# Kernel tuning notes

Hardware: AMD Instinct MI355X
Metric: run time of the kernel (lower is better)

The kernel has to match this reference:

```python
import jax, jax.numpy as jnp
import numpy as np

V, B, T, E, H = 16384, 64, 256, 128, 1024


def setup_inputs() -> dict:
    key = jax.random.key(0)
    ks = jax.random.split(key, 10)
    inp = {
        'input_data': jax.random.randint(ks[0], (B, T), 0, V, dtype=jnp.int32),
        'targets': jax.random.randint(ks[1], (B, T), 0, V, dtype=jnp.int32),
        'embedding': jax.random.normal(ks[2], (V, E), dtype=jnp.float32) * 0.02,
        # layer 1 GRU (input E, hidden H): gate kernel [E+H, 2H], candidate kernel [E+H, H]
        'W_g1': jax.random.normal(ks[3], (E + H, 2 * H), dtype=jnp.float32) * 0.05,
        'b_g1': jnp.ones((2 * H,), dtype=jnp.float32),  # TF GRUCell gate bias init = 1.0
        'W_c1': jax.random.normal(ks[4], (E + H, H), dtype=jnp.float32) * 0.05,
        'b_c1': jnp.zeros((H,), dtype=jnp.float32),
        # layer 2 GRU (input H, hidden H)
        'W_g2': jax.random.normal(ks[5], (2 * H, 2 * H), dtype=jnp.float32) * 0.05,
        'b_g2': jnp.ones((2 * H,), dtype=jnp.float32),
        'W_c2': jax.random.normal(ks[6], (2 * H, H), dtype=jnp.float32) * 0.05,
        'b_c2': jnp.zeros((H,), dtype=jnp.float32),
        'softmax_w': jax.random.normal(ks[7], (H, V), dtype=jnp.float32) * 1e-4,
        'softmax_b': jnp.zeros((V,), dtype=jnp.float32),
    }
    return inp


def _gru_step(h, x, W_g, b_g, W_c, b_c):
    # TF GRUCell: r,u = sigmoid([x,h] @ W_g + b_g); c = tanh([x, r*h] @ W_c + b_c)
    ru = jax.nn.sigmoid(jnp.concatenate([x, h], axis=-1) @ W_g + b_g)
    r, u = jnp.split(ru, 2, axis=-1)
    c = jnp.tanh(jnp.concatenate([x, r * h], axis=-1) @ W_c + b_c)
    return u * h + (1.0 - u) * c


def reference(input_data, targets, embedding, W_g1, b_g1, W_c1, b_c1,
              W_g2, b_g2, W_c2, b_c2, softmax_w, softmax_b):
    # inference path: is_training=False, so dropout wrappers are identity
    x = embedding[input_data]               # [B, T, E]
    xs = jnp.transpose(x, (1, 0, 2))        # [T, B, E] time-major for scan

    h0 = (jnp.zeros((B, H), x.dtype), jnp.zeros((B, H), x.dtype))

    def step(carry, x_t):
        h1, h2 = carry
        h1 = _gru_step(h1, x_t, W_g1, b_g1, W_c1, b_c1)
        h2 = _gru_step(h2, h1, W_g2, b_g2, W_c2, b_c2)
        return (h1, h2), h2

    _, ys = jax.lax.scan(step, h0, xs)      # ys: [T, B, H]
    out = jnp.transpose(ys, (1, 0, 2)).reshape(-1, H)  # [B*T, H] batch-major flatten

    logits = out @ softmax_w + softmax_b    # [B*T, V]
    logp = jax.nn.log_softmax(logits, axis=-1)
    flat_t = targets.reshape(-1)
    nll = -jnp.take_along_axis(logp, flat_t[:, None], axis=1)[:, 0]
    loss = jnp.mean(nll)
    return logits, loss
```

## Files before the change

### kernel.cpp

```cpp
#include <hip/hip_runtime.h>

typedef __bf16 bf16_t;
typedef __bf16 bf16x8 __attribute__((ext_vector_type(8)));
typedef float f32x4 __attribute__((ext_vector_type(4)));
typedef float f32x2 __attribute__((ext_vector_type(2)));
typedef unsigned u32x4 __attribute__((ext_vector_type(4)));

constexpr int kB = 64, kT = 256, kE = 128, kH = 1024, kV = 16384;
constexpr int kBT = kB * kT;

__device__ __forceinline__ void ld16_sc(const void* p, u32x4& d) {
    asm volatile("global_load_dwordx4 %0, %1, off sc0 sc1" : "=v"(d) : "v"(p));
}
__device__ __forceinline__ void ld8_sc(const void* p, f32x2& d) {
    asm volatile("global_load_dwordx2 %0, %1, off sc0 sc1" : "=v"(d) : "v"(p));
}
__device__ __forceinline__ void ld8_c(const void* p, f32x2& d) {
    asm volatile("global_load_dwordx2 %0, %1, off" : "=v"(d) : "v"(p));
}
__device__ __forceinline__ void st4_sc(void* p, unsigned v) {
    asm volatile("global_store_dword %0, %1, off sc0 sc1" :: "v"(p), "v"(v));
}
__device__ __forceinline__ void st8_sc(void* p, f32x2 v) {
    asm volatile("global_store_dwordx2 %0, %1, off sc0 sc1" :: "v"(p), "v"(v));
}
__device__ __forceinline__ unsigned ld_flag(const unsigned* p) {
    unsigned v;
    asm volatile("global_load_dword %0, %1, off sc0 sc1\n\ts_waitcnt vmcnt(0)"
                 : "=v"(v) : "v"(p) : "memory");
    return v;
}
#define WAITVM(n) asm volatile("s_waitcnt vmcnt(" #n ")" ::: "memory")

#define GL2LDS(gp, lp) __builtin_amdgcn_global_load_lds( \
    (const __attribute__((address_space(1))) void*)(gp), \
    (__attribute__((address_space(3))) void*)(lp), 16, 0, 0)

__device__ __forceinline__ unsigned pack_bf16(float a, float b) {
    union { unsigned u; __bf16 h[2]; } c;
    c.h[0] = (__bf16)a; c.h[1] = (__bf16)b;
    return c.u;
}
__device__ __forceinline__ f32x2 mk2(float a, float b) {
    f32x2 v; v[0] = a; v[1] = b; return v;
}

__global__ void zero_bytes(char* p, size_t n) {
    size_t stride = (size_t)gridDim.x * blockDim.x * 16;
    for (size_t i = ((size_t)blockIdx.x * blockDim.x + threadIdx.x) * 16; i < n; i += stride) {
        uint4 z; z.x = z.y = z.z = z.w = 0;
        *reinterpret_cast<uint4*>(p + i) = z;
    }
}

__global__ void transpose_to_bf16(const float* __restrict__ src, bf16_t* __restrict__ dst,
                                  int R, int C) {
    __shared__ float tile[32][33];
    int c0 = blockIdx.x * 32, r0 = blockIdx.y * 32;
    for (int rr = threadIdx.y; rr < 32; rr += 8)
        tile[rr][threadIdx.x] = src[(size_t)(r0 + rr) * C + c0 + threadIdx.x];
    __syncthreads();
    for (int rr = threadIdx.y; rr < 32; rr += 8)
        dst[(size_t)(c0 + rr) * R + r0 + threadIdx.x] = (bf16_t)tile[threadIdx.x][rr];
}

__global__ __launch_bounds__(256) void embed_gather(const int* __restrict__ ids,
                                                    const float* __restrict__ emb,
                                                    bf16_t* __restrict__ XB) {
    int base = blockIdx.x * 16;
    for (int idx = threadIdx.x; idx < 16 * kE; idx += 256) {
        int r = idx >> 7, k = idx & 127;
        int row = base + r;
        XB[(size_t)row * kE + k] = (bf16_t)emb[(size_t)ids[row] * kE + k];
    }
}

__global__ __launch_bounds__(256) void xpre_gemm(
    const bf16_t* __restrict__ XB, const bf16_t* __restrict__ WT,
    const float* __restrict__ bias, float* __restrict__ Cout, int N) {
    __shared__ __align__(16) char As[128 * 256];
    __shared__ __align__(16) char Bs[128 * 256];
    const int tid = threadIdx.x;
    const int w = tid >> 6, l = tid & 63, lr = l & 15, lk8 = (l >> 4) * 8;
    const int wr = w >> 1, wc = w & 1;
    const size_t row0 = (size_t)blockIdx.y * 128, col0 = (size_t)blockIdx.x * 128;
    for (int c = tid; c < 2048; c += 256) {
        int o = c * 16; int row = o >> 8; int kk = o & 255;
        int dst = (row << 8) + (kk ^ ((row & 7) << 4));
        *reinterpret_cast<bf16x8*>(As + dst) =
            *reinterpret_cast<const bf16x8*>(XB + (row0 + row) * kE + (kk >> 1));
        *reinterpret_cast<bf16x8*>(Bs + dst) =
            *reinterpret_cast<const bf16x8*>(WT + (col0 + row) * kE + (kk >> 1));
    }
    __syncthreads();
    f32x4 acc[4][4] = {};
    #pragma unroll
    for (int ks = 0; ks < 4; ++ks) {
        int kb = (ks * 32 + lk8) * 2;
        bf16x8 af[4], bfv[4];
        #pragma unroll
        for (int mf = 0; mf < 4; ++mf) {
            int r = wr * 64 + mf * 16 + lr;
            af[mf] = *reinterpret_cast<const bf16x8*>(As + (r << 8) + (kb ^ ((r & 7) << 4)));
        }
        #pragma unroll
        for (int nf = 0; nf < 4; ++nf) {
            int r = wc * 64 + nf * 16 + lr;
            bfv[nf] = *reinterpret_cast<const bf16x8*>(Bs + (r << 8) + (kb ^ ((r & 7) << 4)));
        }
        #pragma unroll
        for (int mf = 0; mf < 4; ++mf)
            #pragma unroll
            for (int nf = 0; nf < 4; ++nf)
                acc[mf][nf] = __builtin_amdgcn_mfma_f32_16x16x32_bf16(af[mf], bfv[nf], acc[mf][nf], 0, 0, 0);
    }
    #pragma unroll
    for (int mf = 0; mf < 4; ++mf) {
        size_t row = row0 + wr * 64 + mf * 16 + (l >> 4) * 4;
        #pragma unroll
        for (int nf = 0; nf < 4; ++nf) {
            size_t col = col0 + wc * 64 + nf * 16 + lr;
            float bvl = bias[col];
            #pragma unroll
            for (int i = 0; i < 4; ++i)
                Cout[(row + i) * (size_t)N + col] = acc[mf][nf][i] + bvl;
        }
    }
}

struct PP {
    const bf16_t *WG1HT, *WC1HT, *WG2T, *WC2T;
    const float *XG1, *XC1;
    const float *bg2, *bc2;
    float *H1F, *H2F, *U1, *U2;
    bf16_t *X2, *X2C0, *X2C1, *RH1, *YS;
    unsigned *flags;
};

__device__ __forceinline__ void wait_flags(const unsigned* flags, int base, int cnt,
                                           unsigned tgt, int lane) {
    if ((unsigned)lane < (unsigned)cnt) {
        const unsigned* p = flags + (size_t)(base + lane) * 16;
        while (ld_flag(p) < tgt)
            __builtin_amdgcn_s_sleep(1);
    }
}

template<int RBSH>
__device__ __forceinline__ void mm_part(const bf16_t* __restrict__ A, int astr,
                                        const char* __restrict__ wl, int kbase,
                                        int w, int lr, int lk, f32x4 (&acc)[4][2]) {
    const int kbeg = w * 256;
    const bf16_t* base[4];
    #pragma unroll
    for (int mf = 0; mf < 4; ++mf)
        base[mf] = A + (size_t)(mf * 16 + lr) * astr + kbeg + lk;
    u32x4 buf[4][4];
    #pragma unroll
    for (int pi = 0; pi < 4; ++pi)
        #pragma unroll
        for (int mf = 0; mf < 4; ++mf)
            ld16_sc(base[mf] + pi * 32, buf[pi][mf]);
    #pragma unroll
    for (int ki = 0; ki < 8; ++ki) {
        int rem = 7 - ki; if (rem > 3) rem = 3;
        if (rem == 3)      WAITVM(12);
        else if (rem == 2) WAITVM(8);
        else if (rem == 1) WAITVM(4);
        else               WAITVM(0);
        __builtin_amdgcn_sched_barrier(0);
        #pragma unroll
        for (int nf = 0; nf < 2; ++nf) {
            int rr = nf * 16 + lr;
            int kb = (kbase + kbeg + ki * 32 + lk) * 2;
            bf16x8 wv = *reinterpret_cast<const bf16x8*>(wl + (rr << RBSH) + (kb ^ ((rr & 7) << 4)));
            #pragma unroll
            for (int mf = 0; mf < 4; ++mf)
                acc[mf][nf] = __builtin_amdgcn_mfma_f32_16x16x32_bf16(
                    __builtin_bit_cast(bf16x8, buf[ki & 3][mf]), wv, acc[mf][nf], 0, 0, 0);
        }
        if (ki + 4 < 8) {
            #pragma unroll
            for (int mf = 0; mf < 4; ++mf)
                ld16_sc(base[mf] + (ki + 4) * 32, buf[ki & 3][mf]);
        }
    }
}

__global__ __launch_bounds__(256, 1) void rnn_persistent(PP P) {
    __shared__ __align__(16) char wlds[131072];
    __shared__ float red[4][64][8];
    const int blk = blockIdx.x, tid = threadIdx.x;
    const int w = tid >> 6, l = tid & 63, lr = l & 15, lk = (l >> 4) * 8;
    int grp, idx;
    if (blk < 64)       { grp = 0; idx = blk; }
    else if (blk < 96)  { grp = 1; idx = blk - 64; }
    else if (blk < 160) { grp = 2; idx = blk - 96; }
    else                { grp = 3; idx = blk - 160; }
    const int n0 = idx * 32;
    const int K = (grp < 2) ? 1024 : 2048;
    const int rbsh = (grp < 2) ? 11 : 12;
    const bf16_t* Wsrc = (grp == 0) ? P.WG1HT : (grp == 1) ? P.WC1HT : (grp == 2) ? P.WG2T : P.WC2T;

    for (int c = tid; c < (32 * K * 2) / 16; c += 256) {
        int o = c * 16;
        int row = o >> rbsh;
        int kk = o & ((1 << rbsh) - 1);
        bf16x8 v = *reinterpret_cast<const bf16x8*>(Wsrc + (size_t)(n0 + row) * K + (kk >> 1));
        *reinterpret_cast<bf16x8*>(wlds + (row << rbsh) + (kk ^ ((row & 7) << 4))) = v;
    }
    __syncthreads();

    const unsigned* F = P.flags;
    const int r = tid >> 2, cb = (tid & 3) * 2;
    const bool lowhalf = (n0 < 1024);

    f32x2 bx[4], hreg[4];
    #pragma unroll
    for (int p = 0; p < 4; ++p) {
        hreg[p] = mk2(0.f, 0.f);
        int j = n0 + p * 8 + cb;
        if (grp == 2)      bx[p] = *reinterpret_cast<const f32x2*>(P.bg2 + j);
        else if (grp == 3) bx[p] = *reinterpret_cast<const f32x2*>(P.bc2 + j);
    }

    for (int t = 0; t < kT; ++t) {
        unsigned ut = (unsigned)t;
        bf16_t* x2c = (t & 1) ? P.X2C1 : P.X2C0;
        f32x4 acc[4][2] = {};

        if (grp == 0) {
            if (t) wait_flags(F, 64, 32, ut, tid);
            __syncthreads();
            mm_part<11>(P.X2, 2048, wlds, 0, w, lr, lk, acc);
        } else if (grp == 1) {
            wait_flags(F, 0, 64, ut + 1, tid);
            if (t) wait_flags(F, 96, 64, ut, tid - 64);
            if (t >= 2) wait_flags(F, 160, 32, ut - 1, tid - 128);
            __syncthreads();
            mm_part<11>(P.RH1, 1024, wlds, 0, w, lr, lk, acc);
        } else if (grp == 2) {
            if (t) wait_flags(F, 160, 32, ut, tid);
            __syncthreads();
            mm_part<12>(P.X2 + 1024, 2048, wlds, 1024, w, lr, lk, acc);
            wait_flags(F, 64, 32, ut + 1, tid);
            __syncthreads();
            mm_part<12>(P.X2, 2048, wlds, 0, w, lr, lk, acc);
        } else {
            wait_flags(F, 64, 32, ut + 1, tid);
            __syncthreads();
            mm_part<12>(x2c, 2048, wlds, 0, w, lr, lk, acc);
            wait_flags(F, 96, 64, ut + 1, tid);
            __syncthreads();
            mm_part<12>(x2c + 1024, 2048, wlds, 1024, w, lr, lk, acc);
        }

        f32x2 pa[4], px[4];
        if (grp == 0) {
            #pragma unroll
            for (int p = 0; p < 4; ++p) {
                int j = n0 + p * 8 + cb;
                ld8_c(P.XG1 + ((size_t)r * kT + t) * 2048 + j, px[p]);
                if (lowhalf) ld8_sc(P.H1F + r * 1024 + j, pa[p]);
            }
        } else if (grp == 1) {
            #pragma unroll
            for (int p = 0; p < 4; ++p) {
                int j = n0 + p * 8 + cb;
                ld8_c(P.XC1 + ((size_t)r * kT + t) * 1024 + j, px[p]);
                ld8_sc(P.U1 + r * 1024 + j, pa[p]);
            }
        } else if (grp == 2) {
            #pragma unroll
            for (int p = 0; p < 4; ++p) {
                int j = n0 + p * 8 + cb;
                px[p] = bx[p];
                if (lowhalf) ld8_sc(P.H2F + r * 1024 + j, pa[p]);
            }
        } else {
            #pragma unroll
            for (int p = 0; p < 4; ++p) {
                int j = n0 + p * 8 + cb;
                px[p] = bx[p];
                ld8_sc(P.U2 + r * 1024 + j, pa[p]);
            }
        }
        asm volatile("s_waitcnt vmcnt(0)" ::: "memory");
        __builtin_amdgcn_sched_barrier(0);

        #pragma unroll
        for (int p = 0; p < 4; ++p) {
            const int nf = p >> 1;
            if (((l >> 3) & 1) == (p & 1)) {
                #pragma unroll
                for (int mf = 0; mf < 4; ++mf)
                    #pragma unroll
                    for (int i = 0; i < 4; ++i)
                        red[w][mf * 16 + (l >> 4) * 4 + i][l & 7] = acc[mf][nf][i];
            }
            __syncthreads();
            {
                float v0 = red[0][r][cb] + red[1][r][cb] + red[2][r][cb] + red[3][r][cb];
                float v1 = red[0][r][cb + 1] + red[1][r][cb + 1] + red[2][r][cb + 1] + red[3][r][cb + 1];
                int j = n0 + p * 8 + cb;
                v0 += px[p][0]; v1 += px[p][1];
                if (grp == 0) {
                    float g0 = 1.f / (1.f + __expf(-v0));
                    float g1 = 1.f / (1.f + __expf(-v1));
                    if (lowhalf) {
                        st4_sc(P.RH1 + r * 1024 + j, pack_bf16(g0 * pa[p][0], g1 * pa[p][1]));
                    } else {
                        st8_sc(P.U1 + r * 1024 + j - 1024, mk2(g0, g1));
                    }
                } else if (grp == 1) {
                    float cc0 = tanhf(v0), cc1 = tanhf(v1);
                    float hn0 = pa[p][0] * hreg[p][0] + (1.f - pa[p][0]) * cc0;
                    float hn1 = pa[p][1] * hreg[p][1] + (1.f - pa[p][1]) * cc1;
                    hreg[p] = mk2(hn0, hn1);
                    st8_sc(P.H1F + r * 1024 + j, hreg[p]);
                    unsigned pk = pack_bf16(hn0, hn1);
                    st4_sc(P.X2 + r * 2048 + j, pk);
                    st4_sc(x2c + r * 2048 + j, pk);
                } else if (grp == 2) {
                    float g0 = 1.f / (1.f + __expf(-v0));
                    float g1 = 1.f / (1.f + __expf(-v1));
                    if (lowhalf) {
                        st4_sc(x2c + r * 2048 + 1024 + j, pack_bf16(g0 * pa[p][0], g1 * pa[p][1]));
                    } else {
                        st8_sc(P.U2 + r * 1024 + j - 1024, mk2(g0, g1));
                    }
                } else {
                    float cc0 = tanhf(v0), cc1 = tanhf(v1);
                    float hn0 = pa[p][0] * hreg[p][0] + (1.f - pa[p][0]) * cc0;
                    float hn1 = pa[p][1] * hreg[p][1] + (1.f - pa[p][1]) * cc1;
                    hreg[p] = mk2(hn0, hn1);
                    st8_sc(P.H2F + r * 1024 + j, hreg[p]);
                    unsigned pk = pack_bf16(hn0, hn1);
                    st4_sc(P.X2 + r * 2048 + 1024 + j, pk);
                    *reinterpret_cast<unsigned*>(P.YS + ((size_t)r * kT + t) * 1024 + j) = pk;
                }
            }
            __syncthreads();
        }

        asm volatile("s_waitcnt vmcnt(0)" ::: "memory");
        __syncthreads();
        if (tid == 0)
            st4_sc((void*)&F[(size_t)blk * 16], ut + 1);
    }
}

__global__ __launch_bounds__(256) void logits_gemm(
    const bf16_t* __restrict__ Amat,
    const bf16_t* __restrict__ Bt,
    const float* __restrict__ bias,
    float* __restrict__ out) {
    __shared__ __align__(16) bf16_t As[128 * 64];
    __shared__ __align__(16) bf16_t Bs[128 * 64];
    const int tid = threadIdx.x;
    const int w = tid >> 6, l = tid & 63;
    const int wr = w >> 1, wc = w & 1;
    const int lr = l & 15, lk8 = (l >> 4) * 8;
    const int row0 = blockIdx.y * 128, col0 = blockIdx.x * 128;

    int srow[4], scol[4];
    #pragma unroll
    for (int v = 0; v < 4; ++v) {
        int idx = v * 256 + tid;
        srow[v] = idx >> 3;
        scol[v] = (idx & 7) * 8;
    }

    f32x4 acc[4][4] = {};
    for (int kt = 0; kt < 16; ++kt) {
        int ko = kt * 64;
        #pragma unroll
        for (int v = 0; v < 4; ++v) {
            GL2LDS(Amat + (size_t)(row0 + srow[v]) * kH + ko + scol[v], As + srow[v] * 64 + scol[v]);
            GL2LDS(Bt + (size_t)(col0 + srow[v]) * kH + ko + scol[v], Bs + srow[v] * 64 + scol[v]);
        }
        asm volatile("s_waitcnt vmcnt(0)" ::: "memory");
        __syncthreads();
        #pragma unroll
        for (int ks = 0; ks < 2; ++ks) {
            bf16x8 af[4], bfv[4];
            #pragma unroll
            for (int mf = 0; mf < 4; ++mf)
                af[mf] = *reinterpret_cast<const bf16x8*>(As + (wr * 64 + mf * 16 + lr) * 64 + ks * 32 + lk8);
            #pragma unroll
            for (int nf = 0; nf < 4; ++nf)
                bfv[nf] = *reinterpret_cast<const bf16x8*>(Bs + (wc * 64 + nf * 16 + lr) * 64 + ks * 32 + lk8);
            #pragma unroll
            for (int mf = 0; mf < 4; ++mf)
                #pragma unroll
                for (int nf = 0; nf < 4; ++nf)
                    acc[mf][nf] = __builtin_amdgcn_mfma_f32_16x16x32_bf16(af[mf], bfv[nf], acc[mf][nf], 0, 0, 0);
        }
        __syncthreads();
    }
    #pragma unroll
    for (int mf = 0; mf < 4; ++mf) {
        int row = row0 + wr * 64 + mf * 16 + (l >> 4) * 4;
        #pragma unroll
        for (int nf = 0; nf < 4; ++nf) {
            int col = col0 + wc * 64 + nf * 16 + lr;
            float bvl = bias[col];
            #pragma unroll
            for (int i = 0; i < 4; ++i)
                out[(size_t)(row + i) * kV + col] = acc[mf][nf][i] + bvl;
        }
    }
}

__global__ __launch_bounds__(256) void row_nll(const float* __restrict__ logits,
                                               const int* __restrict__ targets,
                                               float* __restrict__ nll) {
    int row = blockIdx.x;
    const float* rowp = logits + (size_t)row * kV;
    int tid = threadIdx.x;
    float m = -1e30f, s = 0.f;
    for (int j = tid; j < kV; j += 256) {
        float v = rowp[j];
        if (v > m) { s = s * __expf(m - v) + 1.f; m = v; }
        else s += __expf(v - m);
    }
    __shared__ float ms[256], ss[256];
    ms[tid] = m; ss[tid] = s;
    __syncthreads();
    for (int off = 128; off; off >>= 1) {
        if (tid < off) {
            float m2 = ms[tid + off], s2 = ss[tid + off];
            float M = fmaxf(ms[tid], m2);
            ss[tid] = ss[tid] * __expf(ms[tid] - M) + s2 * __expf(m2 - M);
            ms[tid] = M;
        }
        __syncthreads();
    }
    if (tid == 0) {
        float lse = ms[0] + __logf(ss[0]);
        nll[row] = lse - rowp[targets[row]];
    }
}

__global__ __launch_bounds__(256) void loss_reduce(const float* __restrict__ nll,
                                                   float* __restrict__ out) {
    __shared__ float sm[256];
    int tid = threadIdx.x;
    float s = 0.f;
    for (int i = tid; i < kBT; i += 256) s += nll[i];
    sm[tid] = s;
    __syncthreads();
    for (int off = 128; off; off >>= 1) {
        if (tid < off) sm[tid] += sm[tid + off];
        __syncthreads();
    }
    if (tid == 0) out[0] = sm[0] / (float)kBT;
}

extern "C" void kernel_launch(void* const* d_in, const int* in_sizes, int n_in,
                              void* d_out, int out_size, void* d_ws, size_t ws_size,
                              hipStream_t stream) {
    const int*   ids = (const int*)d_in[0];
    const int*   tgt = (const int*)d_in[1];
    const float* emb = (const float*)d_in[2];
    const float* Wg1 = (const float*)d_in[3];
    const float* bg1 = (const float*)d_in[4];
    const float* Wc1 = (const float*)d_in[5];
    const float* bc1 = (const float*)d_in[6];
    const float* Wg2 = (const float*)d_in[7];
    const float* bg2 = (const float*)d_in[8];
    const float* Wc2 = (const float*)d_in[9];
    const float* bc2 = (const float*)d_in[10];
    const float* sw  = (const float*)d_in[11];
    const float* sb  = (const float*)d_in[12];
    float* out = (float*)d_out;

    char* ws = (char*)d_ws;
    size_t off = 0;
    auto alloc = [&](size_t bytes) -> void* {
        void* p = ws + off;
        off += (bytes + 255) & ~(size_t)255;
        return p;
    };
    bf16_t* WG1HT = (bf16_t*)alloc((size_t)2048 * 1024 * 2);
    bf16_t* WC1HT = (bf16_t*)alloc((size_t)1024 * 1024 * 2);
    bf16_t* WG2T  = (bf16_t*)alloc((size_t)2048 * 2048 * 2);
    bf16_t* WC2T  = (bf16_t*)alloc((size_t)1024 * 2048 * 2);
    bf16_t* SWT   = (bf16_t*)alloc((size_t)kV * kH * 2);
    bf16_t* WG1XT = (bf16_t*)alloc((size_t)2048 * kE * 2);
    bf16_t* WC1XT = (bf16_t*)alloc((size_t)1024 * kE * 2);
    bf16_t* XB    = (bf16_t*)alloc((size_t)kBT * kE * 2);
    float*  XG1   = (float*)alloc((size_t)kBT * 2048 * 4);
    float*  XC1   = (float*)alloc((size_t)kBT * 1024 * 4);
    bf16_t* YS    = (bf16_t*)alloc((size_t)kBT * kH * 2);
    float*  NLL   = (float*)alloc((size_t)kBT * 4);
    char*   zbase = ws + off;
    float*  H1F   = (float*)alloc((size_t)kB * kH * 4);
    float*  H2F   = (float*)alloc((size_t)kB * kH * 4);
    float*  U1    = (float*)alloc((size_t)kB * kH * 4);
    float*  U2    = (float*)alloc((size_t)kB * kH * 4);
    bf16_t* X2    = (bf16_t*)alloc((size_t)kB * 2048 * 2);
    bf16_t* X2C0  = (bf16_t*)alloc((size_t)kB * 2048 * 2);
    bf16_t* X2C1  = (bf16_t*)alloc((size_t)kB * 2048 * 2);
    bf16_t* RH1   = (bf16_t*)alloc((size_t)kB * kH * 2);
    unsigned* FLAGS = (unsigned*)alloc(192 * 16 * 4);
    size_t zlen = (ws + off) - zbase;

    transpose_to_bf16<<<dim3(64, 32), dim3(32, 8), 0, stream>>>(Wg1 + (size_t)kE * 2048, WG1HT, 1024, 2048);
    transpose_to_bf16<<<dim3(32, 32), dim3(32, 8), 0, stream>>>(Wc1 + (size_t)kE * 1024, WC1HT, 1024, 1024);
    transpose_to_bf16<<<dim3(64, 64), dim3(32, 8), 0, stream>>>(Wg2, WG2T, 2048, 2048);
    transpose_to_bf16<<<dim3(32, 64), dim3(32, 8), 0, stream>>>(Wc2, WC2T, 2048, 1024);
    transpose_to_bf16<<<dim3(512, 32), dim3(32, 8), 0, stream>>>(sw, SWT, 1024, 16384);
    transpose_to_bf16<<<dim3(64, 4), dim3(32, 8), 0, stream>>>(Wg1, WG1XT, 128, 2048);
    transpose_to_bf16<<<dim3(32, 4), dim3(32, 8), 0, stream>>>(Wc1, WC1XT, 128, 1024);

    embed_gather<<<kBT / 16, 256, 0, stream>>>(ids, emb, XB);
    xpre_gemm<<<dim3(16, kBT / 128), 256, 0, stream>>>(XB, WG1XT, bg1, XG1, 2048);
    xpre_gemm<<<dim3(8, kBT / 128), 256, 0, stream>>>(XB, WC1XT, bc1, XC1, 1024);
    zero_bytes<<<256, 256, 0, stream>>>(zbase, zlen);

    PP prm;
    prm.WG1HT = WG1HT; prm.WC1HT = WC1HT; prm.WG2T = WG2T; prm.WC2T = WC2T;
    prm.XG1 = XG1; prm.XC1 = XC1; prm.bg2 = bg2; prm.bc2 = bc2;
    prm.H1F = H1F; prm.H2F = H2F; prm.U1 = U1; prm.U2 = U2;
    prm.X2 = X2; prm.X2C0 = X2C0; prm.X2C1 = X2C1; prm.RH1 = RH1; prm.YS = YS;
    prm.flags = FLAGS;
    void* args[] = { &prm };
    hipLaunchCooperativeKernel((const void*)rnn_persistent, dim3(192), dim3(256), args, 0, stream);

    logits_gemm<<<dim3(kV / 128, kBT / 128), 256, 0, stream>>>(YS, SWT, sb, out);
    row_nll<<<kBT, 256, 0, stream>>>(out, tgt, NLL);
    loss_reduce<<<1, 256, 0, stream>>>(NLL, out + (size_t)kBT * kV);
}
```

Measured before the change: 6.315 ms.

## Fuse partial log-softmax into logits GEMM epilogue and remap block order

The logits GEMM epilogue now computes, per row and 64-column chunk, a partial max and sum-of-exp using lane shuffles and writes them to a small buffer. A lightweight finalize kernel then merges the 256 partials per row and gathers the target logit, so the full 1 GB logits array is no longer reread. The GEMM block index is also swizzled to change the tile visit order, likely for cache locality. Separately, the layer-1 RNN group now defers two flag waits until after its first matmul, overlapping that wait with compute.

Result: faster. 6.158 ms (-2.5%).

```diff
diff --git a/kernel.cpp b/kernel.cpp
--- a/kernel.cpp
+++ b/kernel.cpp
@@ -235,10 +235,11 @@
             mm_part<11>(P.X2, 2048, wlds, 0, w, lr, lk, acc);
         } else if (grp == 1) {
             wait_flags(F, 0, 64, ut + 1, tid);
-            if (t) wait_flags(F, 96, 64, ut, tid - 64);
-            if (t >= 2) wait_flags(F, 160, 32, ut - 1, tid - 128);
             __syncthreads();
             mm_part<11>(P.RH1, 1024, wlds, 0, w, lr, lk, acc);
+            if (t) wait_flags(F, 96, 64, ut, tid);
+            if (t >= 2) wait_flags(F, 160, 32, ut - 1, tid - 64);
+            __syncthreads();
         } else if (grp == 2) {
             if (t) wait_flags(F, 160, 32, ut, tid);
             __syncthreads();
@@ -354,14 +355,17 @@
     const bf16_t* __restrict__ Amat,
     const bf16_t* __restrict__ Bt,
     const float* __restrict__ bias,
-    float* __restrict__ out) {
+    float* __restrict__ out,
+    float* __restrict__ PM) {
     __shared__ __align__(16) bf16_t As[128 * 64];
     __shared__ __align__(16) bf16_t Bs[128 * 64];
     const int tid = threadIdx.x;
     const int w = tid >> 6, l = tid & 63;
     const int wr = w >> 1, wc = w & 1;
     const int lr = l & 15, lk8 = (l >> 4) * 8;
-    const int row0 = blockIdx.y * 128, col0 = blockIdx.x * 128;
+    int lin = blockIdx.y * gridDim.x + blockIdx.x;
+    int s = (lin & 7) * 2048 + (lin >> 3);
+    const int row0 = (s >> 7) * 128, col0 = (s & 127) * 128;
 
     int srow[4], scol[4];
     #pragma unroll
@@ -398,48 +402,51 @@
         }
         __syncthreads();
     }
+    const int chunk = (col0 >> 6) + wc;
     #pragma unroll
     for (int mf = 0; mf < 4; ++mf) {
-        int row = row0 + wr * 64 + mf * 16 + (l >> 4) * 4;
-        #pragma unroll
-        for (int nf = 0; nf < 4; ++nf) {
-            int col = col0 + wc * 64 + nf * 16 + lr;
-            float bvl = bias[col];
-            #pragma unroll
-            for (int i = 0; i < 4; ++i)
-                out[(size_t)(row + i) * kV + col] = acc[mf][nf][i] + bvl;
-        }
-    }
-}
-
-__global__ __launch_bounds__(256) void row_nll(const float* __restrict__ logits,
-                                               const int* __restrict__ targets,
-                                               float* __restrict__ nll) {
-    int row = blockIdx.x;
-    const float* rowp = logits + (size_t)row * kV;
-    int tid = threadIdx.x;
+        #pragma unroll
+        for (int i = 0; i < 4; ++i) {
+            int row = row0 + wr * 64 + mf * 16 + (l >> 4) * 4 + i;
+            float vals[4];
+            #pragma unroll
+            for (int nf = 0; nf < 4; ++nf) {
+                int col = col0 + wc * 64 + nf * 16 + lr;
+                vals[nf] = acc[mf][nf][i] + bias[col];
+                out[(size_t)row * kV + col] = vals[nf];
+            }
+            float m = fmaxf(fmaxf(vals[0], vals[1]), fmaxf(vals[2], vals[3]));
+            float sm = __expf(vals[0] - m) + __expf(vals[1] - m)
+                     + __expf(vals[2] - m) + __expf(vals[3] - m);
+            #pragma unroll
+            for (int d = 1; d < 16; d <<= 1) {
+                float m2 = __shfl_xor(m, d);
+                float s2 = __shfl_xor(sm, d);
+                float M = fmaxf(m, m2);
+                sm = sm * __expf(m - M) + s2 * __expf(m2 - M);
+                m = M;
+            }
+            if (lr == 0)
+                *reinterpret_cast<f32x2*>(PM + ((size_t)chunk * kBT + row) * 2) = mk2(m, sm);
+        }
+    }
+}
+
+__global__ __launch_bounds__(256) void nll_finalize(const float* __restrict__ PM,
+                                                    const float* __restrict__ logits,
+                                                    const int* __restrict__ targets,
+                                                    float* __restrict__ nll) {
+    int row = blockIdx.x * 256 + threadIdx.x;
     float m = -1e30f, s = 0.f;
-    for (int j = tid; j < kV; j += 256) {
-        float v = rowp[j];
-        if (v > m) { s = s * __expf(m - v) + 1.f; m = v; }
-        else s += __expf(v - m);
-    }
-    __shared__ float ms[256], ss[256];
-    ms[tid] = m; ss[tid] = s;
-    __syncthreads();
-    for (int off = 128; off; off >>= 1) {
-        if (tid < off) {
-            float m2 = ms[tid + off], s2 = ss[tid + off];
-            float M = fmaxf(ms[tid], m2);
-            ss[tid] = ss[tid] * __expf(ms[tid] - M) + s2 * __expf(m2 - M);
-            ms[tid] = M;
-        }
-        __syncthreads();
-    }
-    if (tid == 0) {
-        float lse = ms[0] + __logf(ss[0]);
-        nll[row] = lse - rowp[targets[row]];
-    }
+    #pragma unroll 4
+    for (int c = 0; c < 256; ++c) {
+        f32x2 p = *reinterpret_cast<const f32x2*>(PM + ((size_t)c * kBT + row) * 2);
+        float M = fmaxf(m, p[0]);
+        s = s * __expf(m - M) + p[1] * __expf(p[0] - M);
+        m = M;
+    }
+    float tl = logits[(size_t)row * kV + targets[row]];
+    nll[row] = m + __logf(s) - tl;
 }
 
 __global__ __launch_bounds__(256) void loss_reduce(const float* __restrict__ nll,
@@ -494,6 +501,7 @@
     float*  XC1   = (float*)alloc((size_t)kBT * 1024 * 4);
     bf16_t* YS    = (bf16_t*)alloc((size_t)kBT * kH * 2);
     float*  NLL   = (float*)alloc((size_t)kBT * 4);
+    float*  PM    = (float*)alloc((size_t)256 * kBT * 2 * 4);
     char*   zbase = ws + off;
     float*  H1F   = (float*)alloc((size_t)kB * kH * 4);
     float*  H2F   = (float*)alloc((size_t)kB * kH * 4);
@@ -528,7 +536,7 @@
     void* args[] = { &prm };
     hipLaunchCooperativeKernel((const void*)rnn_persistent, dim3(192), dim3(256), args, 0, stream);
 
-    logits_gemm<<<dim3(kV / 128, kBT / 128), 256, 0, stream>>>(YS, SWT, sb, out);
-    row_nll<<<kBT, 256, 0, stream>>>(out, tgt, NLL);
+    logits_gemm<<<dim3(kV / 128, kBT / 128), 256, 0, stream>>>(YS, SWT, sb, out, PM);
+    nll_finalize<<<kBT / 256, 256, 0, stream>>>(PM, out, tgt, NLL);
     loss_reduce<<<1, 256, 0, stream>>>(NLL, out + (size_t)kBT * kV);
 }
```
